# Kernel tuning notes

Hardware: AMD Instinct MI355X
Metric: run time of the kernel (lower is better)

## Reference

```python
import jax, jax.numpy as jnp
import numpy as np

HIDDEN = 1024
NUM_HEAD = 16
HEAD_DIM = HIDDEN // NUM_HEAD
B, S = 2, 2048


def setup_inputs() -> dict:
    key = jax.random.key(0)
    ks = jax.random.split(key, 9)
    scale = 1.0 / np.sqrt(HIDDEN)
    X = jax.random.normal(ks[0], (B, S, HIDDEN), dtype=jnp.float32)
    # causal mask, broadcastable over heads: [B, 1, S, S]
    causal = jnp.tril(jnp.ones((S, S), dtype=jnp.int32))
    mask = jnp.broadcast_to(causal[None, None, :, :], (B, 1, S, S))
    Wq = jax.random.normal(ks[1], (HIDDEN, HIDDEN), dtype=jnp.float32) * scale
    bq = jnp.zeros((HIDDEN,), dtype=jnp.float32)
    Wk = jax.random.normal(ks[2], (HIDDEN, HIDDEN), dtype=jnp.float32) * scale
    bk = jnp.zeros((HIDDEN,), dtype=jnp.float32)
    Wv = jax.random.normal(ks[3], (HIDDEN, HIDDEN), dtype=jnp.float32) * scale
    bv = jnp.zeros((HIDDEN,), dtype=jnp.float32)
    Wo = jax.random.normal(ks[4], (HIDDEN, HIDDEN), dtype=jnp.float32) * scale
    bo = jnp.zeros((HIDDEN,), dtype=jnp.float32)
    return {"X": X, "mask": mask, "Wq": Wq, "bq": bq, "Wk": Wk, "bk": bk,
            "Wv": Wv, "bv": bv, "Wo": Wo, "bo": bo}


def reference(X, mask, Wq, bq, Wk, bk, Wv, bv, Wo, bo):
    bsz, seq_len, _ = X.shape
    # Q/K/V projections (torch Linear: x @ W.T + b; here W stored as [in, out])
    Q = X @ Wq + bq
    K = X @ Wk + bk
    V = X @ Wv + bv
    # [B, H, S, D]
    Q = Q.reshape(bsz, seq_len, NUM_HEAD, HEAD_DIM).transpose(0, 2, 1, 3)
    K = K.reshape(bsz, seq_len, NUM_HEAD, HEAD_DIM).transpose(0, 2, 1, 3)
    V = V.reshape(bsz, seq_len, NUM_HEAD, HEAD_DIM).transpose(0, 2, 1, 3)
    # scores: [B, H, S, S]
    scores = jnp.einsum('bhqd,bhkd->bhqk', Q, K) / jnp.sqrt(
        jnp.asarray(HEAD_DIM, dtype=X.dtype))
    scores = jnp.where(mask == 0, jnp.asarray(-jnp.inf, dtype=scores.dtype), scores)
    # dropout (rate=0.0) is identity; softmax over keys
    attn = jax.nn.softmax(scores, axis=-1)
    out = jnp.einsum('bhqk,bhkd->bhqd', attn, V)
    out = out.transpose(0, 2, 1, 3).reshape(bsz, seq_len, HIDDEN)
    return out @ Wo + bo
```

## Files before the change

kernel.cpp:

```cpp
#include <hip/hip_runtime.h>
#include <stdint.h>

#define HID 1024
#define SEQ 2048
#define NB 2
#define NH 16
#define HD 64
#define MROWS 4096

typedef float f32x4 __attribute__((ext_vector_type(4)));
typedef short s16x4 __attribute__((ext_vector_type(4)));
typedef short s16x8 __attribute__((ext_vector_type(8)));
typedef uint32_t u32x4 __attribute__((ext_vector_type(4)));

#define MFMA16(a, b, c) __builtin_amdgcn_mfma_f32_16x16x32_bf16((a), (b), (c), 0, 0, 0)

#define GLOAD_LDS16(gp, lp)                                                    \
  __builtin_amdgcn_global_load_lds(                                            \
      (const __attribute__((address_space(1))) unsigned int*)(gp),             \
      (__attribute__((address_space(3))) unsigned int*)(lp), 16, 0, 0)

__device__ __forceinline__ short f2bf(float x) {
  uint32_t u = __builtin_bit_cast(uint32_t, x);
  u += 0x7fffu + ((u >> 16) & 1u);
  return (short)(u >> 16);
}

__device__ __forceinline__ uint32_t cvtpk(float lo, float hi) {
  uint32_t r;
  asm("v_cvt_pk_bf16_f32 %0, %1, %2" : "=v"(r) : "v"(lo), "v"(hi));
  return r;
}

__global__ __launch_bounds__(256) void prep_kernel(
    const float* __restrict__ X, const float* __restrict__ w0,
    const float* __restrict__ w1, const float* __restrict__ w2,
    const float* __restrict__ w3, short* __restrict__ Xb,
    short* __restrict__ Wtall) {
  const int z = blockIdx.z;
  if (z == 4) {
    const size_t i = ((size_t)blockIdx.y * 32 + blockIdx.x) * 256 + threadIdx.x;
    const float* s = X + i * 16;
    short* d = Xb + i * 16;
#pragma unroll
    for (int h = 0; h < 2; h++) {
      f32x4 a = *(const f32x4*)(s + h * 8);
      f32x4 b = *(const f32x4*)(s + h * 8 + 4);
      s16x8 o;
      o[0] = f2bf(a[0]); o[1] = f2bf(a[1]); o[2] = f2bf(a[2]); o[3] = f2bf(a[3]);
      o[4] = f2bf(b[0]); o[5] = f2bf(b[1]); o[6] = f2bf(b[2]); o[7] = f2bf(b[3]);
      *(s16x8*)(d + h * 8) = o;
    }
    return;
  }
  __shared__ float t[32][33];
  const float* src = (z == 0) ? w0 : (z == 1) ? w1 : (z == 2) ? w2 : w3;
  short* dst = Wtall + ((size_t)z << 20);
  const int tx = threadIdx.x & 31, ty = threadIdx.x >> 5;
  const int r0 = blockIdx.y * 32, c0 = blockIdx.x * 32;
#pragma unroll
  for (int i = 0; i < 4; i++)
    t[ty + i * 8][tx] = src[(size_t)(r0 + ty + i * 8) * HID + c0 + tx];
  __syncthreads();
#pragma unroll
  for (int i = 0; i < 4; i++)
    dst[(size_t)(c0 + ty + i * 8) * HID + r0 + tx] = f2bf(t[tx][ty + i * 8]);
}

template <int EPI, int MI>
__global__ __launch_bounds__(256) void gemm_bf16(
    const short* __restrict__ A, const short* __restrict__ Bt,
    const float* __restrict__ b0, const float* __restrict__ b1,
    const float* __restrict__ b2, short* __restrict__ Qb, short* __restrict__ Kg,
    short* __restrict__ Vg, float* __restrict__ Out) {
  __shared__ char lds[MI * 2048 + 8192];
  const int tid = threadIdx.x;
  const int w = tid >> 6, l = tid & 63, lg = l >> 4, ln = l & 15;
  const int wm = w >> 1, wn = w & 1;
  const int m0 = blockIdx.y * (32 * MI), n0 = blockIdx.x * 128;

  f32x4 acc[MI][4];
#pragma unroll
  for (int i = 0; i < MI; i++)
#pragma unroll
    for (int j = 0; j < 4; j++) acc[i][j] = f32x4{0.f, 0.f, 0.f, 0.f};

  for (int k0 = 0; k0 < 1024; k0 += 32) {
    __syncthreads();
#pragma unroll
    for (int i = 0; i < MI / 2; i++) {
      const int c = i * 256 + tid;
      const int row = c >> 2;
      const int cs = (c & 3) ^ (row & 3);
      GLOAD_LDS16(A + (size_t)(m0 + row) * 1024 + k0 + cs * 8, lds + c * 16);
    }
#pragma unroll
    for (int i = 0; i < 2; i++) {
      const int c = i * 256 + tid;
      const int row = c >> 2;
      const int cs = (c & 3) ^ (row & 3);
      GLOAD_LDS16(Bt + (size_t)(n0 + row) * 1024 + k0 + cs * 8,
                  lds + MI * 2048 + c * 16);
    }
    __syncthreads();

    s16x8 af[MI], bfr[4];
#pragma unroll
    for (int mi = 0; mi < MI; mi++) {
      const int row = wm * (16 * MI) + mi * 16 + ln;
      af[mi] = *(const s16x8*)(lds + row * 64 + ((lg ^ (row & 3)) * 16));
    }
#pragma unroll
    for (int ni = 0; ni < 4; ni++) {
      const int row = wn * 64 + ni * 16 + ln;
      bfr[ni] =
          *(const s16x8*)(lds + MI * 2048 + row * 64 + ((lg ^ (row & 3)) * 16));
    }
#pragma unroll
    for (int mi = 0; mi < MI; mi++)
#pragma unroll
      for (int ni = 0; ni < 4; ni++)
        acc[mi][ni] = MFMA16(af[mi], bfr[ni], acc[mi][ni]);
  }

  const float QSC = 0.18033688011112042f;
#pragma unroll
  for (int ni = 0; ni < 4; ni++) {
    const int c = n0 + wn * 64 + ni * 16 + ln;
    if (EPI == 0) {
      const int mat = c >> 10, cc = c & 1023, hh = cc >> 6, d = cc & 63;
      const float* bp = (mat == 0) ? b0 : (mat == 1) ? b1 : b2;
      const float bias = bp[cc];
#pragma unroll
      for (int mi = 0; mi < MI; mi++) {
#pragma unroll
        for (int r = 0; r < 4; r++) {
          const int m = m0 + wm * (16 * MI) + mi * 16 + lg * 4 + r;
          const int bb = m >> 11, s = m & 2047;
          const float fv = acc[mi][ni][r] + bias;
          const size_t bh = (size_t)(bb * 16 + hh);
          if (mat == 0) {
            Qb[(bh * SEQ + s) * HD + d] = f2bf(fv * QSC);
          } else if (mat == 1) {
            const int tile = s >> 6, rr = s & 63;
            Kg[bh * (SEQ * HD) + tile * 4096 + rr * 64 +
               ((((d >> 3) ^ (rr & 7)) << 3) | (d & 7))] = f2bf(fv);
          } else {
            const int sp = (s & ~31) | ((s & 12) << 1) | (((s >> 4) & 1) << 2) |
                           (s & 3);
            const int tile = sp >> 6, kp = sp & 63;
            Vg[bh * (SEQ * HD) + tile * 4096 + d * 64 +
               ((((kp >> 3) ^ (d & 7)) << 3) | (kp & 7))] = f2bf(fv);
          }
        }
      }
    } else {
      const float bias = b0[c];
#pragma unroll
      for (int mi = 0; mi < MI; mi++)
#pragma unroll
        for (int r = 0; r < 4; r++) {
          const int m = m0 + wm * (16 * MI) + mi * 16 + lg * 4 + r;
          Out[(size_t)m * 1024 + c] = acc[mi][ni][r] + bias;
        }
    }
  }
}


__device__ __forceinline__ void stage_tile(const short* Kt, const short* Vt,
                                           int t, char* buf, int w, int l) {
  const char* src = (w < 2) ? ((const char*)(Kt + (size_t)t * 4096) + (w & 1) * 4096)
                            : ((const char*)(Vt + (size_t)t * 4096) + (w & 1) * 4096);
  char* dst = buf + ((w < 2) ? 0 : 8192) + (w & 1) * 4096;
#pragma unroll
  for (int j = 0; j < 4; j++)
    GLOAD_LDS16(src + j * 1024 + l * 16, dst + j * 1024);
}

template <bool MASK>
__device__ __forceinline__ void softmax_pv(f32x4 st[4], const s16x8 vf[2][4],
                                           const s16x8& ones, f32x4 o[4],
                                           float& m2, float& l_run, int k0,
                                           int qrow, int lg) {
  float p[4][4];
#pragma unroll
  for (int mt = 0; mt < 4; mt++)
#pragma unroll
    for (int r = 0; r < 4; r++) {
      float v = st[mt][r];
      if (MASK) {
        const int key = k0 + mt * 16 + lg * 4 + r;
        if (key > qrow) v = -3e38f;
      }
      p[mt][r] = v;
    }
  float a0 = fmaxf(fmaxf(p[0][0], p[0][1]), fmaxf(p[0][2], p[0][3]));
  float a1 = fmaxf(fmaxf(p[1][0], p[1][1]), fmaxf(p[1][2], p[1][3]));
  float a2 = fmaxf(fmaxf(p[2][0], p[2][1]), fmaxf(p[2][2], p[2][3]));
  float a3 = fmaxf(fmaxf(p[3][0], p[3][1]), fmaxf(p[3][2], p[3][3]));
  float pmax = fmaxf(fmaxf(a0, a1), fmaxf(a2, a3));

  if (!__all(pmax <= m2 + 8.0f)) {
    pmax = fmaxf(pmax, __shfl_xor(pmax, 16));
    pmax = fmaxf(pmax, __shfl_xor(pmax, 32));
    const float m_new = fmaxf(m2, pmax);
    const float corr = exp2f(m2 - m_new);
    l_run *= corr;
#pragma unroll
    for (int i = 0; i < 4; i++) o[i] *= corr;
    m2 = m_new;
  }
#pragma unroll
  for (int mt = 0; mt < 4; mt++)
#pragma unroll
    for (int r = 0; r < 4; r++) p[mt][r] = exp2f(p[mt][r] - m2);

  s16x8 pf[2];
#pragma unroll
  for (int s = 0; s < 2; s++) {
    u32x4 wv;
    wv[0] = cvtpk(p[s * 2][0], p[s * 2][1]);
    wv[1] = cvtpk(p[s * 2][2], p[s * 2][3]);
    wv[2] = cvtpk(p[s * 2 + 1][0], p[s * 2 + 1][1]);
    wv[3] = cvtpk(p[s * 2 + 1][2], p[s * 2 + 1][3]);
    pf[s] = __builtin_bit_cast(s16x8, wv);
  }
  f32x4 ps = f32x4{0.f, 0.f, 0.f, 0.f};
  ps = MFMA16(ones, pf[0], ps);
  ps = MFMA16(ones, pf[1], ps);
#pragma unroll
  for (int s = 0; s < 2; s++)
#pragma unroll
    for (int vmt = 0; vmt < 4; vmt++)
      o[vmt] = MFMA16(vf[s][vmt], pf[s], o[vmt]);
  l_run += ps[0];
}

template <bool MASK>
__device__ __forceinline__ void compute_tile(const char* cbuf, const s16x8& qf0,
                                             const s16x8& qf1, const s16x8& ones,
                                             int k0, int qrow, int lg, int ln,
                                             float& m2, float& l_run, f32x4 o[4]) {
  const int x = ln & 7;
  f32x4 st[4];
#pragma unroll
  for (int mt = 0; mt < 4; mt++) {
    const char* rowp = cbuf + (mt * 16 + ln) * 128;
    const s16x8 k0f = *(const s16x8*)(rowp + ((lg ^ x) * 16));
    const s16x8 k1f = *(const s16x8*)(rowp + (((4 + lg) ^ x) * 16));
    st[mt] = f32x4{0.f, 0.f, 0.f, 0.f};
    st[mt] = MFMA16(k0f, qf0, st[mt]);
    st[mt] = MFMA16(k1f, qf1, st[mt]);
  }
  s16x8 vf[2][4];
#pragma unroll
  for (int s = 0; s < 2; s++)
#pragma unroll
    for (int vmt = 0; vmt < 4; vmt++)
      vf[s][vmt] = *(const s16x8*)(cbuf + 8192 + (vmt * 16 + ln) * 128 +
                                   (((s * 4 + lg) ^ x) * 16));
  softmax_pv<MASK>(st, vf, ones, o, m2, l_run, k0, qrow, lg);
}

__device__ __forceinline__ void attn_group_pass(const short* Kt, const short* Vt,
                                                const short* __restrict__ Qb,
                                                short* __restrict__ Ob, int bh,
                                                int G, int w, int l, char* lds) {
  const int lg = l >> 4, ln = l & 15;
  const int qrow = G * 64 + w * 16 + ln;
  const short* Qp = Qb + ((size_t)bh * SEQ + qrow) * HD;
  const s16x8 qf0 = *(const s16x8*)(Qp + lg * 8);
  const s16x8 qf1 = *(const s16x8*)(Qp + 32 + lg * 8);
  s16x8 ones;
#pragma unroll
  for (int j = 0; j < 8; j++) ones[j] = (short)0x3F80;

  float m2 = -3e38f, l_run = 0.f;
  f32x4 o[4];
#pragma unroll
  for (int i = 0; i < 4; i++) o[i] = f32x4{0.f, 0.f, 0.f, 0.f};

  const int nt = G + 1;
  stage_tile(Kt, Vt, 0, lds, w, l);
  for (int t = 0; t < nt - 1; ++t) {
    stage_tile(Kt, Vt, t + 1, lds + ((t + 1) & 1) * 16384, w, l);
    asm volatile("s_waitcnt vmcnt(4)" ::: "memory");
    __builtin_amdgcn_s_barrier();
    __builtin_amdgcn_sched_barrier(0);
    compute_tile<false>(lds + (t & 1) * 16384, qf0, qf1, ones, t * 64, qrow, lg,
                        ln, m2, l_run, o);
    __builtin_amdgcn_s_barrier();
    __builtin_amdgcn_sched_barrier(0);
  }
  asm volatile("s_waitcnt vmcnt(0)" ::: "memory");
  __builtin_amdgcn_s_barrier();
  __builtin_amdgcn_sched_barrier(0);
  compute_tile<true>(lds + ((nt - 1) & 1) * 16384, qf0, qf1, ones, (nt - 1) * 64,
                     qrow, lg, ln, m2, l_run, o);
  __builtin_amdgcn_s_barrier();
  __builtin_amdgcn_sched_barrier(0);

  const float inv = 1.0f / l_run;
  const int bb = bh >> 4, hh = bh & 15;
  const size_t orow = (size_t)(bb * SEQ + qrow) * HID + hh * HD;
#pragma unroll
  for (int mt = 0; mt < 4; mt++) {
    s16x4 ov;
#pragma unroll
    for (int r = 0; r < 4; r++) ov[r] = f2bf(o[mt][r] * inv);
    *(s16x4*)(Ob + orow + mt * 16 + lg * 4) = ov;
  }
}

__global__ __launch_bounds__(256) void attn_kernel(const short* __restrict__ Qb,
                                                   const short* __restrict__ Kg,
                                                   const short* __restrict__ Vg,
                                                   short* __restrict__ Ob) {
  __shared__ char lds[32768];
  const int bid = blockIdx.x;
  const int L = (bid & 7) * 64 + (bid >> 3);
  const int bh = L >> 4, g = L & 15;
  const int w = threadIdx.x >> 6, l = threadIdx.x & 63;
  const short* Kt = Kg + (size_t)bh * (SEQ * HD);
  const short* Vt = Vg + (size_t)bh * (SEQ * HD);
  attn_group_pass(Kt, Vt, Qb, Ob, bh, g, w, l, lds);
  attn_group_pass(Kt, Vt, Qb, Ob, bh, 31 - g, w, l, lds);
}

extern "C" void kernel_launch(void* const* d_in, const int* in_sizes, int n_in,
                              void* d_out, int out_size, void* d_ws,
                              size_t ws_size, hipStream_t stream) {
  const float* X = (const float*)d_in[0];
  const float* Wq = (const float*)d_in[2];
  const float* bq = (const float*)d_in[3];
  const float* Wk = (const float*)d_in[4];
  const float* bk = (const float*)d_in[5];
  const float* Wv = (const float*)d_in[6];
  const float* bv = (const float*)d_in[7];
  const float* Wo = (const float*)d_in[8];
  const float* bo = (const float*)d_in[9];
  float* out = (float*)d_out;

  char* ws = (char*)d_ws;
  short* Xb = (short*)(ws);
  short* Wtall = (short*)(ws + (8u << 20));
  short* Qb = (short*)(ws + (16u << 20));
  short* Kg = (short*)(ws + (24u << 20));
  short* Vg = (short*)(ws + (32u << 20));
  short* Ob = (short*)(ws + (40u << 20));
  short* Wto = Wtall + (3u << 20);

  prep_kernel<<<dim3(32, 32, 5), 256, 0, stream>>>(X, Wq, Wk, Wv, Wo, Xb, Wtall);

  gemm_bf16<0, 4><<<dim3(24, 32), 256, 0, stream>>>(Xb, Wtall, bq, bk, bv, Qb,
                                                    Kg, Vg, nullptr);
  attn_kernel<<<512, 256, 0, stream>>>(Qb, Kg, Vg, Ob);
  gemm_bf16<1, 2><<<dim3(8, 64), 256, 0, stream>>>(Ob, Wto, bo, nullptr, nullptr,
                                                   nullptr, nullptr, nullptr,
                                                   out);
}
```

Baseline: 227.0 us.

## Double-buffer LDS in bf16 GEMM to overlap global loads with MFMA

```diff
diff --git a/kernel.cpp b/kernel.cpp
--- a/kernel.cpp
+++ b/kernel.cpp
@@ -73,7 +73,7 @@
     const float* __restrict__ b0, const float* __restrict__ b1,
     const float* __restrict__ b2, short* __restrict__ Qb, short* __restrict__ Kg,
     short* __restrict__ Vg, float* __restrict__ Out) {
-  __shared__ char lds[MI * 2048 + 8192];
+  __shared__ char lds[2][MI * 2048 + 8192];
   const int tid = threadIdx.x;
   const int w = tid >> 6, l = tid & 63, lg = l >> 4, ln = l & 15;
   const int wm = w >> 1, wn = w & 1;
@@ -85,14 +85,14 @@
 #pragma unroll
     for (int j = 0; j < 4; j++) acc[i][j] = f32x4{0.f, 0.f, 0.f, 0.f};
 
-  for (int k0 = 0; k0 < 1024; k0 += 32) {
-    __syncthreads();
+  auto stage = [&](int buf, int k0) {
 #pragma unroll
     for (int i = 0; i < MI / 2; i++) {
       const int c = i * 256 + tid;
       const int row = c >> 2;
       const int cs = (c & 3) ^ (row & 3);
-      GLOAD_LDS16(A + (size_t)(m0 + row) * 1024 + k0 + cs * 8, lds + c * 16);
+      GLOAD_LDS16(A + (size_t)(m0 + row) * 1024 + k0 + cs * 8,
+                  lds[buf] + c * 16);
     }
 #pragma unroll
     for (int i = 0; i < 2; i++) {
@@ -100,27 +100,46 @@
       const int row = c >> 2;
       const int cs = (c & 3) ^ (row & 3);
       GLOAD_LDS16(Bt + (size_t)(n0 + row) * 1024 + k0 + cs * 8,
-                  lds + MI * 2048 + c * 16);
-    }
-    __syncthreads();
-
+                  lds[buf] + MI * 2048 + c * 16);
+    }
+  };
+
+  stage(0, 0);
+  for (int kt = 0; kt < 32; ++kt) {
+    const int cur = kt & 1;
+    if (kt < 31) {
+      stage(cur ^ 1, (kt + 1) * 32);
+      if constexpr (MI == 4)
+        asm volatile("s_waitcnt vmcnt(4)" ::: "memory");
+      else
+        asm volatile("s_waitcnt vmcnt(3)" ::: "memory");
+    } else {
+      asm volatile("s_waitcnt vmcnt(0)" ::: "memory");
+    }
+    __builtin_amdgcn_s_barrier();
+    __builtin_amdgcn_sched_barrier(0);
+
+    const char* ldsc = lds[cur];
     s16x8 af[MI], bfr[4];
 #pragma unroll
     for (int mi = 0; mi < MI; mi++) {
       const int row = wm * (16 * MI) + mi * 16 + ln;
-      af[mi] = *(const s16x8*)(lds + row * 64 + ((lg ^ (row & 3)) * 16));
+      af[mi] = *(const s16x8*)(ldsc + row * 64 + ((lg ^ (row & 3)) * 16));
     }
 #pragma unroll
     for (int ni = 0; ni < 4; ni++) {
       const int row = wn * 64 + ni * 16 + ln;
       bfr[ni] =
-          *(const s16x8*)(lds + MI * 2048 + row * 64 + ((lg ^ (row & 3)) * 16));
+          *(const s16x8*)(ldsc + MI * 2048 + row * 64 + ((lg ^ (row & 3)) * 16));
     }
 #pragma unroll
     for (int mi = 0; mi < MI; mi++)
 #pragma unroll
       for (int ni = 0; ni < 4; ni++)
         acc[mi][ni] = MFMA16(af[mi], bfr[ni], acc[mi][ni]);
+
+    __builtin_amdgcn_s_barrier();
+    __builtin_amdgcn_sched_barrier(0);
   }
 
   const float QSC = 0.18033688011112042f;
```

Measured after the change: 212.6 us. -6.3%, faster.
